# Optimization experiments

Hardware: AMD Instinct MI355X
Metric: run time of the kernel (lower is better)

Reference implementation:

```python
import jax, jax.numpy as jnp
import numpy as np

HEADS = 4
HID = 610
KER = 50  # cov2KerSize
NEG_SLOPE = 0.2


def gat_layer(x, src, dst, w, b, att_src, att_dst, n_nodes):
    # x: [N, Fin], w: [HEADS*HID, Fin], att_*: [1, HEADS, HID], b: [HID]
    h = (x @ w.T).reshape(n_nodes, HEADS, HID)               # [N,H,D]
    a_src = (h * att_src).sum(-1)                            # [N,H]
    a_dst = (h * att_dst).sum(-1)                            # [N,H]
    alpha = jax.nn.leaky_relu(a_src[src] + a_dst[dst], NEG_SLOPE)  # [E,H]
    # softmax over edges grouped by destination node
    m = jax.ops.segment_max(alpha, dst, num_segments=n_nodes)
    e = jnp.exp(alpha - m[dst])
    denom = jax.ops.segment_sum(e, dst, num_segments=n_nodes)
    a = e / (denom[dst] + 1e-16)                             # [E,H]
    msg = h[src] * a[:, :, None]                             # [E,H,D]
    out = jax.ops.segment_sum(msg, dst, num_segments=n_nodes)  # [N,H,D]
    return out.mean(axis=1) + b                              # [N,D] (concat=False)


def setup_inputs() -> dict:
    key = jax.random.key(0)
    ks = jax.random.split(key, 16)
    N, E, FIN, NOUT = 20000, 100000, 128, 86
    x = jax.random.normal(ks[0], (N, FIN), dtype=jnp.float32)
    edge_index = jax.random.randint(ks[1], (2, E), 0, N, dtype=jnp.int64)
    def kaiming(k, shape, fan_in):
        return jax.random.normal(k, shape, dtype=jnp.float32) * np.float32(np.sqrt(2.0 / fan_in))
    w0 = kaiming(ks[2], (HEADS * HID, FIN), FIN)
    b0 = jnp.zeros((HID,), jnp.float32)
    att_src0 = kaiming(ks[3], (1, HEADS, HID), HID)
    att_dst0 = kaiming(ks[4], (1, HEADS, HID), HID)
    w2 = kaiming(ks[5], (HEADS * HID, HID), HID)
    b2 = jnp.zeros((HID,), jnp.float32)
    att_src1 = kaiming(ks[6], (1, HEADS, HID), HID)
    att_dst1 = kaiming(ks[7], (1, HEADS, HID), HID)
    w4 = kaiming(ks[8], (1, 1, 2, KER), 2 * KER)
    b4 = jnp.zeros((1,), jnp.float32)
    w6 = kaiming(ks[9], (1, 1, KER), KER)
    b6 = jnp.zeros((1,), jnp.float32)
    w8 = kaiming(ks[10], (NOUT, 512), 512)
    b8 = jnp.zeros((NOUT,), jnp.float32)
    return dict(x=x, edge_index=edge_index, w0=w0, b0=b0, att_src0=att_src0,
                att_dst0=att_dst0, w2=w2, b2=b2, att_src1=att_src1,
                att_dst1=att_dst1, w4=w4, b4=b4, w6=w6, b6=b6, w8=w8, b8=b8)


def reference(x, edge_index, w0, b0, att_src0, att_dst0, w2, b2, att_src1,
              att_dst1, w4, b4, w6, b6, w8, b8):
    N = x.shape[0]
    src, dst = edge_index[0], edge_index[1]
    x1 = jax.nn.relu(gat_layer(x, src, dst, w0, b0, att_src0, att_dst0, N))
    x2 = jax.nn.relu(gat_layer(x1, src, dst, w2, b2, att_src1, att_dst1, N))
    # edge features: cat(src_feat, dst_feat) viewed as [E,1,2,HID]
    ef = jnp.stack([x2[src], x2[dst]], axis=1)[:, None, :, :]  # [E,1,2,HID]
    y = jax.lax.conv_general_dilated(ef, w4, (1, 1), 'VALID',
                                     dimension_numbers=('NCHW', 'OIHW', 'NCHW'))
    y = jax.nn.relu(y + b4[None, :, None, None])               # [E,1,1,561]
    y = y.reshape(-1, HID - KER + 1, 1).transpose(0, 2, 1)     # [E,1,561]
    y = jax.lax.conv_general_dilated(y, w6, (1,), 'VALID',
                                     dimension_numbers=('NCH', 'OIH', 'NCH'))
    y = jax.nn.relu(y + b6[None, :, None])                     # [E,1,512]
    # adaptive_avg_pool1d to 512 is identity since length is already 512
    y = y.reshape(-1, 512)
    return y @ w8.T + b8                                       # [E, num_outputs]
```

## Files before the change

kernel.cpp:

```cpp
#include <hip/hip_runtime.h>
#include <math.h>

#define HEADS 4
#define HID 610
#define HIDP 640
#define FIN 128
#define KER 50
#define NOUT 86
#define NEG_SLOPE 0.2f

#define Y1S 616
#define ZSS 520

typedef short bf8_t __attribute__((ext_vector_type(8)));
typedef float f4_t __attribute__((ext_vector_type(4)));

__device__ __forceinline__ ushort f2bf(float f) {
    unsigned u = __float_as_uint(f);
    unsigned r = (u + 0x7FFFu + ((u >> 16) & 1u)) >> 16;
    return (ushort)r;
}
__device__ __forceinline__ ushort f2bf_t(float f) {
    return (ushort)(__float_as_uint(f) >> 16);
}
__device__ __forceinline__ float bf2f(ushort b) { return __uint_as_float(((unsigned)b) << 16); }

__global__ void fill_val(float* __restrict__ p, float v, long n) {
    long i = (long)blockIdx.x * blockDim.x + threadIdx.x;
    if (i < n) p[i] = v;
}

__global__ void copy_int(const int* __restrict__ a, int* __restrict__ b, int n) {
    int i = blockIdx.x * blockDim.x + threadIdx.x;
    if (i < n) b[i] = a[i];
}

__global__ void hist_k(const int* __restrict__ ei, int* __restrict__ hist, int E) {
    int e = blockIdx.x * blockDim.x + threadIdx.x;
    if (e < E) atomicAdd(&hist[ei[E + e]], 1);
}

__global__ __launch_bounds__(1024) void scan_k(const int* __restrict__ hist,
                                               int* __restrict__ base, int Nn) {
    __shared__ int tmp[1024];
    __shared__ int carry;
    if (threadIdx.x == 0) carry = 0;
    __syncthreads();
    for (int c0 = 0; c0 < Nn; c0 += 1024) {
        int i = c0 + threadIdx.x;
        int v = (i < Nn) ? hist[i] : 0;
        tmp[threadIdx.x] = v;
        __syncthreads();
        for (int off = 1; off < 1024; off <<= 1) {
            int t = (threadIdx.x >= off) ? tmp[threadIdx.x - off] : 0;
            __syncthreads();
            tmp[threadIdx.x] += t;
            __syncthreads();
        }
        if (i < Nn) base[i] = carry + tmp[threadIdx.x] - v;
        __syncthreads();
        if (threadIdx.x == 1023) carry += tmp[1023];
        __syncthreads();
    }
    if (threadIdx.x == 0) base[Nn] = carry;
}

__global__ void scatter_k(const int* __restrict__ ei, int* __restrict__ cursor,
                          int* __restrict__ esrc, int* __restrict__ edst,
                          int* __restrict__ eorg, int E) {
    int e = blockIdx.x * blockDim.x + threadIdx.x;
    if (e >= E) return;
    int d = ei[E + e];
    int pos = atomicAdd(&cursor[d], 1);
    esrc[pos] = ei[e];
    edst[pos] = d;
    eorg[pos] = e;
}

__global__ void split_pad(const float* __restrict__ in, ushort* __restrict__ hi,
                          ushort* __restrict__ lo, int R, int K, int Kp) {
    long i = (long)blockIdx.x * blockDim.x + threadIdx.x;
    if (i >= (long)R * Kp) return;
    int r = (int)(i / Kp), c = (int)(i % Kp);
    float v = (c < K) ? in[(long)r * K + c] : 0.f;
    ushort h = f2bf(v);
    hi[i] = h;
    lo[i] = f2bf(v - bf2f(h));
}

__global__ void build_toeplitz(const float* __restrict__ w4, const float* __restrict__ w6,
                               ushort* __restrict__ T) {
    int i = blockIdx.x * blockDim.x + threadIdx.x;
    if (i >= 18 * 512) return;
    int e = i & 7;
    int lane = (i >> 3) & 63;
    int f = i >> 9;
    int n = lane & 15;
    int k = ((lane >> 4) << 3) + e;
    float wv;
    int hilo;
    if (f < 12) {
        int c = f % 3, hc = f / 3;
        int ch = hc & 1;
        hilo = hc >> 1;
        int d = c * 32 + k - n;
        wv = (d >= 0 && d < KER) ? w4[ch * KER + d] : 0.f;
    } else {
        int r2 = f - 12;
        int c = r2 % 3;
        hilo = r2 / 3;
        int d = c * 32 + k - n;
        wv = (d >= 0 && d < KER) ? w6[d] : 0.f;
    }
    ushort h = f2bf(wv);
    T[i] = hilo ? f2bf(wv - bf2f(h)) : h;
}

template <int AMODE, bool BIAS>
__global__ __launch_bounds__(256) void gemm_mfma(const float* __restrict__ A,
                                                 const ushort* __restrict__ Aghi,
                                                 const ushort* __restrict__ Aglo,
                                                 const ushort* __restrict__ Bghi,
                                                 const ushort* __restrict__ Bglo,
                                                 const float* __restrict__ bias,
                                                 float* __restrict__ C,
                                                 int M, int N, int Kp) {
    __shared__ __align__(16) ushort Ah[128 * 32];
    __shared__ __align__(16) ushort Al[128 * 32];
    __shared__ __align__(16) ushort Bh[128 * 32];
    __shared__ __align__(16) ushort Bl[128 * 32];
    int tid = threadIdx.x;
    int wave = tid >> 6, lane = tid & 63;
    int quad = lane >> 4, l16 = lane & 15;
    int wm = wave & 1, wn = wave >> 1;
    int row0 = blockIdx.y * 128, col0 = blockIdx.x * 128;

    float4 pa0[4];
    uint4 pah[2], pal[2], pbh[2], pbl[2];

    auto loadA = [&](int k0) {
        if (AMODE == 0) {
#pragma unroll
            for (int q = 0; q < 4; q++) {
                int p = tid + q * 256;
                int r = p >> 3, c4 = (p & 7) << 2;
                int gr = row0 + r;
                pa0[q] = (gr < M) ? *(const float4*)(A + (size_t)gr * Kp + k0 + c4)
                                  : make_float4(0.f, 0.f, 0.f, 0.f);
            }
        } else {
#pragma unroll
            for (int q = 0; q < 2; q++) {
                int p = tid + q * 256;
                int r = p >> 2, c = p & 3;
                int gr = row0 + r;
                if (gr < M) {
                    pah[q] = *(const uint4*)(Aghi + (size_t)gr * Kp + k0 + c * 8);
                    pal[q] = *(const uint4*)(Aglo + (size_t)gr * Kp + k0 + c * 8);
                } else {
                    pah[q] = make_uint4(0, 0, 0, 0);
                    pal[q] = make_uint4(0, 0, 0, 0);
                }
            }
        }
    };
    auto loadB = [&](int k0) {
#pragma unroll
        for (int q = 0; q < 2; q++) {
            int p = tid + q * 256;
            int r = p >> 2, c = p & 3;
            int gr = col0 + r;
            if (gr < N) {
                pbh[q] = *(const uint4*)(Bghi + (size_t)gr * Kp + k0 + c * 8);
                pbl[q] = *(const uint4*)(Bglo + (size_t)gr * Kp + k0 + c * 8);
            } else {
                pbh[q] = make_uint4(0, 0, 0, 0);
                pbl[q] = make_uint4(0, 0, 0, 0);
            }
        }
    };
    auto writeLDS = [&]() {
        if (AMODE == 0) {
#pragma unroll
            for (int q = 0; q < 4; q++) {
                int p = tid + q * 256;
                int r = p >> 3, m = p & 7;
                int pos = r * 32 + ((((m >> 1)) ^ ((r >> 1) & 3)) << 3) + ((m & 1) << 2);
                float4 v = pa0[q];
                ushort4 hv, lv;
                hv.x = f2bf(v.x); lv.x = f2bf(v.x - bf2f(hv.x));
                hv.y = f2bf(v.y); lv.y = f2bf(v.y - bf2f(hv.y));
                hv.z = f2bf(v.z); lv.z = f2bf(v.z - bf2f(hv.z));
                hv.w = f2bf(v.w); lv.w = f2bf(v.w - bf2f(hv.w));
                *(ushort4*)&Ah[pos] = hv;
                *(ushort4*)&Al[pos] = lv;
            }
        } else {
#pragma unroll
            for (int q = 0; q < 2; q++) {
                int p = tid + q * 256;
                int r = p >> 2, c = p & 3;
                int pos = r * 32 + ((c ^ ((r >> 1) & 3)) << 3);
                *(uint4*)&Ah[pos] = pah[q];
                *(uint4*)&Al[pos] = pal[q];
            }
        }
#pragma unroll
        for (int q = 0; q < 2; q++) {
            int p = tid + q * 256;
            int r = p >> 2, c = p & 3;
            int pos = r * 32 + ((c ^ ((r >> 1) & 3)) << 3);
            *(uint4*)&Bh[pos] = pbh[q];
            *(uint4*)&Bl[pos] = pbl[q];
        }
    };

    f4_t acc[4][4];
#pragma unroll
    for (int i = 0; i < 4; i++)
#pragma unroll
        for (int j = 0; j < 4; j++) acc[i][j] = (f4_t){0.f, 0.f, 0.f, 0.f};

    loadA(0);
    loadB(0);
    int sw = (quad ^ ((l16 >> 1) & 3)) << 3;
    for (int k0 = 0; k0 < Kp; k0 += 32) {
        __syncthreads();
        writeLDS();
        __syncthreads();
        if (k0 + 32 < Kp) {
            loadA(k0 + 32);
            loadB(k0 + 32);
        }
        bf8_t ah[4], al[4], bh[4], bl[4];
#pragma unroll
        for (int t = 0; t < 4; t++) {
            int ar = wm * 64 + t * 16 + l16;
            ah[t] = *(const bf8_t*)&Ah[ar * 32 + sw];
            al[t] = *(const bf8_t*)&Al[ar * 32 + sw];
            int br = wn * 64 + t * 16 + l16;
            bh[t] = *(const bf8_t*)&Bh[br * 32 + sw];
            bl[t] = *(const bf8_t*)&Bl[br * 32 + sw];
        }
#pragma unroll
        for (int i = 0; i < 4; i++)
#pragma unroll
            for (int j = 0; j < 4; j++) {
                acc[i][j] = __builtin_amdgcn_mfma_f32_16x16x32_bf16(ah[i], bh[j], acc[i][j], 0, 0, 0);
                acc[i][j] = __builtin_amdgcn_mfma_f32_16x16x32_bf16(al[i], bh[j], acc[i][j], 0, 0, 0);
                acc[i][j] = __builtin_amdgcn_mfma_f32_16x16x32_bf16(ah[i], bl[j], acc[i][j], 0, 0, 0);
            }
    }
#pragma unroll
    for (int i = 0; i < 4; i++) {
#pragma unroll
        for (int r = 0; r < 4; r++) {
            int grow = row0 + wm * 64 + i * 16 + quad * 4 + r;
            if (grow >= M) continue;
#pragma unroll
            for (int j = 0; j < 4; j++) {
                int gcol = col0 + wn * 64 + j * 16 + l16;
                if (gcol >= N) continue;
                float v = acc[i][j][r];
                if (BIAS) v += bias[gcol];
                C[(size_t)grow * N + gcol] = v;
            }
        }
    }
}

__global__ __launch_bounds__(256) void attn_dots(const float* __restrict__ h,
                                                 const float* __restrict__ att_s,
                                                 const float* __restrict__ att_d,
                                                 float* __restrict__ a_src,
                                                 float* __restrict__ a_dst, int Nn) {
    int n = blockIdx.x;
    int head = threadIdx.x >> 6;
    int lane = threadIdx.x & 63;
    const float2* hr = (const float2*)(h + (long)n * (HEADS * HID) + head * HID);
    const float2* as = (const float2*)(att_s + head * HID);
    const float2* ad = (const float2*)(att_d + head * HID);
    float ss = 0.f, sd = 0.f;
    for (int d = lane; d < HID / 2; d += 64) {
        float2 hv = hr[d], av = as[d], dv = ad[d];
        ss += hv.x * av.x + hv.y * av.y;
        sd += hv.x * dv.x + hv.y * dv.y;
    }
    for (int off = 32; off > 0; off >>= 1) {
        ss += __shfl_down(ss, off);
        sd += __shfl_down(sd, off);
    }
    if (lane == 0) {
        a_src[n * HEADS + head] = ss;
        a_dst[n * HEADS + head] = sd;
    }
}

template <int OUTMODE>
__global__ __launch_bounds__(256) void node_aggregate(
    const float* __restrict__ h, const float* __restrict__ asrc,
    const float* __restrict__ adst, const int* __restrict__ base,
    const int* __restrict__ esrc, const float* __restrict__ bias,
    float* __restrict__ xout, ushort* __restrict__ xhi, ushort* __restrict__ xlo,
    int Nn) {
    int wave = threadIdx.x >> 6, lane = threadIdx.x & 63;
    int n = blockIdx.x * 4 + wave;
    if (n >= Nn) return;
    int b0 = base[n], deg = base[n + 1] - b0;
    float ad[HEADS];
#pragma unroll
    for (int hh = 0; hh < HEADS; hh++) ad[hh] = adst[n * HEADS + hh];
    float m[HEADS] = {-INFINITY, -INFINITY, -INFINITY, -INFINITY};
    for (int eb = 0; eb < deg; eb += 64) {
        int i = eb + lane;
        if (i < deg) {
            int s = esrc[b0 + i];
#pragma unroll
            for (int hh = 0; hh < HEADS; hh++) {
                float v = asrc[s * HEADS + hh] + ad[hh];
                v = v >= 0.f ? v : NEG_SLOPE * v;
                m[hh] = fmaxf(m[hh], v);
            }
        }
    }
#pragma unroll
    for (int off = 32; off > 0; off >>= 1)
#pragma unroll
        for (int hh = 0; hh < HEADS; hh++) m[hh] = fmaxf(m[hh], __shfl_xor(m[hh], off));
    float sden[HEADS] = {0.f, 0.f, 0.f, 0.f};
    for (int eb = 0; eb < deg; eb += 64) {
        int i = eb + lane;
        if (i < deg) {
            int s = esrc[b0 + i];
#pragma unroll
            for (int hh = 0; hh < HEADS; hh++) {
                float v = asrc[s * HEADS + hh] + ad[hh];
                v = v >= 0.f ? v : NEG_SLOPE * v;
                sden[hh] += expf(v - m[hh]);
            }
        }
    }
#pragma unroll
    for (int off = 32; off > 0; off >>= 1)
#pragma unroll
        for (int hh = 0; hh < HEADS; hh++) sden[hh] += __shfl_xor(sden[hh], off);
    float inv[HEADS];
#pragma unroll
    for (int hh = 0; hh < HEADS; hh++) inv[hh] = 0.25f / (sden[hh] + 1e-16f);
    float acc0[10] = {}, acc1[10] = {}, acc2[10] = {}, acc3[10] = {};
    for (int eb = 0; eb < deg; eb += 64) {
        int i = eb + lane;
        int sreg = 0;
        float coef[HEADS] = {0.f, 0.f, 0.f, 0.f};
        if (i < deg) {
            sreg = esrc[b0 + i];
#pragma unroll
            for (int hh = 0; hh < HEADS; hh++) {
                float v = asrc[sreg * HEADS + hh] + ad[hh];
                v = v >= 0.f ? v : NEG_SLOPE * v;
                coef[hh] = expf(v - m[hh]) * inv[hh];
            }
        }
        int cnt = deg - eb < 64 ? deg - eb : 64;
        for (int j = 0; j < cnt; j++) {
            int s = __shfl(sreg, j);
            float c0 = __shfl(coef[0], j), c1 = __shfl(coef[1], j);
            float c2 = __shfl(coef[2], j), c3 = __shfl(coef[3], j);
            const float* hr = h + (size_t)s * (HEADS * HID);
#pragma unroll
            for (int t = 0; t < 10; t++) {
                int d = lane + t * 64;
                if (d < HID) {
                    acc0[t] = fmaf(c0, hr[d], acc0[t]);
                    acc1[t] = fmaf(c1, hr[HID + d], acc1[t]);
                    acc2[t] = fmaf(c2, hr[2 * HID + d], acc2[t]);
                    acc3[t] = fmaf(c3, hr[3 * HID + d], acc3[t]);
                }
            }
        }
    }
#pragma unroll
    for (int t = 0; t < 10; t++) {
        int d = lane + t * 64;
        if (d < HID) {
            float v = acc0[t] + acc1[t] + acc2[t] + acc3[t] + bias[d];
            v = v > 0.f ? v : 0.f;
            if (OUTMODE == 0) {
                xout[(size_t)n * HIDP + d] = v;
            } else {
                ushort hv = f2bf(v);
                xhi[(size_t)n * HIDP + d] = hv;
                xlo[(size_t)n * HIDP + d] = f2bf(v - bf2f(hv));
            }
        }
    }
    for (int d = HID + lane; d < HIDP; d += 64) {
        if (OUTMODE == 0) {
            xout[(size_t)n * HIDP + d] = 0.f;
        } else {
            xhi[(size_t)n * HIDP + d] = 0;
            xlo[(size_t)n * HIDP + d] = 0;
        }
    }
}

__global__ __launch_bounds__(256, 3) void edge_fused(
    const ushort* __restrict__ x2hi, const ushort* __restrict__ x2lo,
    const int* __restrict__ esrc, const int* __restrict__ edst,
    const int* __restrict__ eorg, const ushort* __restrict__ T,
    const float* __restrict__ b4, const float* __restrict__ b6,
    const ushort* __restrict__ w8hi, const ushort* __restrict__ w8lo,
    const float* __restrict__ b8, float* __restrict__ out, int E) {
    __shared__ __align__(16) ushort y1h[16 * Y1S];
    __shared__ __align__(16) ushort y1l[16 * Y1S];
    const int tid = threadIdx.x;
    const int wave = tid >> 6, lane = tid & 63;
    const int quad = lane >> 4, l16 = lane & 15;
    const int e0 = blockIdx.x * 16;
    const int p = wave & 1;
    const int half = wave >> 1;
    const int p16 = p * 16;

    int i = e0 + l16;
    if (i >= E) i = E - 1;
    const int s = esrc[i], d = edst[i];
    const ushort* psh = x2hi + (size_t)s * HIDP + quad * 8;
    const ushort* psl = x2lo + (size_t)s * HIDP + quad * 8;
    const ushort* pth = x2hi + (size_t)d * HIDP + quad * 8;
    const ushort* ptl = x2lo + (size_t)d * HIDP + quad * 8;

    bf8_t Wsh[6], Wsl[6], Wth[6], Wtl[6];
#define LDCH(slot, m)                                     \
    {                                                     \
        const int o_ = p16 + 32 * (m);                    \
        Wsh[slot] = *(const bf8_t*)(psh + o_);            \
        Wth[slot] = *(const bf8_t*)(pth + o_);            \
        if ((m) <= 18) {                                  \
            Wsl[slot] = *(const bf8_t*)(psl + o_);        \
            Wtl[slot] = *(const bf8_t*)(ptl + o_);        \
        }                                                 \
    }
    const int t0 = half * 9;
#pragma unroll
    for (int m = 0; m < 5; m++) LDCH(m, t0 + m);

    for (int idx = tid; idx < 16 * (Y1S - 576); idx += 256) {
        int r = idx / (Y1S - 576);
        int j = 576 + (idx - r * (Y1S - 576));
        y1h[r * Y1S + j] = 0;
        y1l[r * Y1S + j] = 0;
    }

    bf8_t B1h[2][3], B1l[2][2];
#pragma unroll
    for (int ch = 0; ch < 2; ch++) {
#pragma unroll
        for (int c = 0; c < 3; c++)
            B1h[ch][c] = *(const bf8_t*)&T[(ch * 3 + c) * 512 + lane * 8];
#pragma unroll
        for (int c = 0; c < 2; c++)
            B1l[ch][c] = *(const bf8_t*)&T[((2 + ch) * 3 + c) * 512 + lane * 8];
    }
    const float bb4 = b4[0], bb6 = b6[0];

#pragma unroll
    for (int tt = 0; tt < 9; tt++) {
        if (tt <= 5) LDCH((tt + 5) % 6, t0 + tt + 5);
        const int c0 = tt % 6, c1 = (tt + 1) % 6, c2 = (tt + 2) % 6;
        f4_t acc = {bb4, bb4, bb4, bb4};
        acc = __builtin_amdgcn_mfma_f32_16x16x32_bf16(Wsh[c0], B1h[0][0], acc, 0, 0, 0);
        acc = __builtin_amdgcn_mfma_f32_16x16x32_bf16(Wsl[c0], B1h[0][0], acc, 0, 0, 0);
        acc = __builtin_amdgcn_mfma_f32_16x16x32_bf16(Wsh[c0], B1l[0][0], acc, 0, 0, 0);
        acc = __builtin_amdgcn_mfma_f32_16x16x32_bf16(Wth[c0], B1h[1][0], acc, 0, 0, 0);
        acc = __builtin_amdgcn_mfma_f32_16x16x32_bf16(Wtl[c0], B1h[1][0], acc, 0, 0, 0);
        acc = __builtin_amdgcn_mfma_f32_16x16x32_bf16(Wth[c0], B1l[1][0], acc, 0, 0, 0);
        acc = __builtin_amdgcn_mfma_f32_16x16x32_bf16(Wsh[c1], B1h[0][1], acc, 0, 0, 0);
        acc = __builtin_amdgcn_mfma_f32_16x16x32_bf16(Wsl[c1], B1h[0][1], acc, 0, 0, 0);
        acc = __builtin_amdgcn_mfma_f32_16x16x32_bf16(Wsh[c1], B1l[0][1], acc, 0, 0, 0);
        acc = __builtin_amdgcn_mfma_f32_16x16x32_bf16(Wth[c1], B1h[1][1], acc, 0, 0, 0);
        acc = __builtin_amdgcn_mfma_f32_16x16x32_bf16(Wtl[c1], B1h[1][1], acc, 0, 0, 0);
        acc = __builtin_amdgcn_mfma_f32_16x16x32_bf16(Wth[c1], B1l[1][1], acc, 0, 0, 0);
        acc = __builtin_amdgcn_mfma_f32_16x16x32_bf16(Wsh[c2], B1h[0][2], acc, 0, 0, 0);
        acc = __builtin_amdgcn_mfma_f32_16x16x32_bf16(Wth[c2], B1h[1][2], acc, 0, 0, 0);
        const int j0 = p16 + 32 * (t0 + tt);
#pragma unroll
        for (int r = 0; r < 4; r++) {
            int e_ = quad * 4 + r;
            int pos = e_ * Y1S + j0 + l16;
            float v = acc[r];
            v = v > 0.f ? v : 0.f;
            ushort hh = f2bf_t(v);
            y1h[pos] = hh;
            y1l[pos] = f2bf(v - bf2f(hh));
        }
    }
    __syncthreads();

    bf8_t B2h[3], B2l[2];
#pragma unroll
    for (int c = 0; c < 3; c++) B2h[c] = *(const bf8_t*)&T[(12 + c) * 512 + lane * 8];
#pragma unroll
    for (int c = 0; c < 2; c++) B2l[c] = *(const bf8_t*)&T[(15 + c) * 512 + lane * 8];
    const int arow1 = l16 * Y1S + quad * 8;
    bf8_t Yh[4], Yl[4];
#define LDY(slot, m)                                          \
    {                                                         \
        const int o_ = arow1 + p16 + 32 * (m);                \
        Yh[slot] = *(const bf8_t*)&y1h[o_];                   \
        if ((m) <= 16) Yl[slot] = *(const bf8_t*)&y1l[o_];    \
    }
    const int t0b = half * 8;
#pragma unroll
    for (int m = 0; m < 3; m++) LDY(m, t0b + m);
    f4_t zac[8];
#pragma unroll
    for (int tt = 0; tt < 8; tt++) {
        if (tt <= 6) LDY((tt + 3) & 3, t0b + tt + 3);
        const int c0 = tt & 3, c1 = (tt + 1) & 3, c2 = (tt + 2) & 3;
        f4_t acc = {bb6, bb6, bb6, bb6};
        acc = __builtin_amdgcn_mfma_f32_16x16x32_bf16(Yh[c0], B2h[0], acc, 0, 0, 0);
        acc = __builtin_amdgcn_mfma_f32_16x16x32_bf16(Yl[c0], B2h[0], acc, 0, 0, 0);
        acc = __builtin_amdgcn_mfma_f32_16x16x32_bf16(Yh[c0], B2l[0], acc, 0, 0, 0);
        acc = __builtin_amdgcn_mfma_f32_16x16x32_bf16(Yh[c1], B2h[1], acc, 0, 0, 0);
        acc = __builtin_amdgcn_mfma_f32_16x16x32_bf16(Yl[c1], B2h[1], acc, 0, 0, 0);
        acc = __builtin_amdgcn_mfma_f32_16x16x32_bf16(Yh[c1], B2l[1], acc, 0, 0, 0);
        acc = __builtin_amdgcn_mfma_f32_16x16x32_bf16(Yh[c2], B2h[2], acc, 0, 0, 0);
#pragma unroll
        for (int r = 0; r < 4; r++) {
            float v = acc[r];
            zac[tt][r] = v > 0.f ? v : 0.f;
        }
    }
    __syncthreads();

#pragma unroll
    for (int tt = 0; tt < 8; tt++) {
        const int j02 = p16 + 32 * (t0b + tt);
#pragma unroll
        for (int r = 0; r < 4; r++) {
            int e_ = quad * 4 + r;
            int pos = e_ * ZSS + j02 + l16;
            float v = zac[tt][r];
            ushort hh = f2bf_t(v);
            y1h[pos] = hh;
            y1l[pos] = f2bf(v - bf2f(hh));
        }
    }
    __syncthreads();

#pragma unroll
    for (int it = 0; it < 2; it++) {
        const int nt = wave + it * 4;
        if (nt < 6) {
            const int col = nt * 16 + l16;
            const int wrow = col < NOUT ? col : 0;
            const float bias = col < NOUT ? b8[col] : 0.f;
            f4_t acc = {bias, bias, bias, bias};
            const int arow = l16 * ZSS + quad * 8;
            const ushort* wph = w8hi + (size_t)wrow * 512 + quad * 8;
            const ushort* wpl = w8lo + (size_t)wrow * 512 + quad * 8;
#pragma unroll
            for (int c = 0; c < 16; c++) {
                bf8_t zh = *(const bf8_t*)&y1h[arow + c * 32];
                bf8_t zl = *(const bf8_t*)&y1l[arow + c * 32];
                bf8_t wh = *(const bf8_t*)(wph + c * 32);
                bf8_t wl = *(const bf8_t*)(wpl + c * 32);
                acc = __builtin_amdgcn_mfma_f32_16x16x32_bf16(zh, wh, acc, 0, 0, 0);
                acc = __builtin_amdgcn_mfma_f32_16x16x32_bf16(zl, wh, acc, 0, 0, 0);
                acc = __builtin_amdgcn_mfma_f32_16x16x32_bf16(zh, wl, acc, 0, 0, 0);
            }
            if (col < NOUT) {
#pragma unroll
                for (int r = 0; r < 4; r++) {
                    int er = e0 + quad * 4 + r;
                    if (er < E) out[(size_t)eorg[er] * NOUT + col] = acc[r];
                }
            }
        }
    }
#undef LDCH
#undef LDY
}

extern "C" void kernel_launch(void* const* d_in, const int* in_sizes, int n_in,
                              void* d_out, int out_size, void* d_ws, size_t ws_size,
                              hipStream_t stream) {
    const float* x = (const float*)d_in[0];
    const int* ei = (const int*)d_in[1];
    const float* w0 = (const float*)d_in[2];
    const float* b0 = (const float*)d_in[3];
    const float* att_s0 = (const float*)d_in[4];
    const float* att_d0 = (const float*)d_in[5];
    const float* w2 = (const float*)d_in[6];
    const float* b2 = (const float*)d_in[7];
    const float* att_s1 = (const float*)d_in[8];
    const float* att_d1 = (const float*)d_in[9];
    const float* w4 = (const float*)d_in[10];
    const float* b4 = (const float*)d_in[11];
    const float* w6 = (const float*)d_in[12];
    const float* b6 = (const float*)d_in[13];
    const float* w8 = (const float*)d_in[14];
    const float* b8 = (const float*)d_in[15];
    float* out = (float*)d_out;

    const int Nn = in_sizes[0] / FIN;
    const int E = in_sizes[1] / 2;
    const int HD = HEADS * HID;

    float* ws = (float*)d_ws;
    size_t o = 0;
    float* buf1 = ws + o; o += (size_t)Nn * HIDP;
    ushort* x1hi = (ushort*)buf1;
    ushort* x1lo = x1hi + (size_t)Nn * HIDP;
    ushort* w8hi = (ushort*)(ws + o);
    ushort* w8lo = w8hi + (size_t)NOUT * 512; o += (size_t)NOUT * 512;
    int* base = (int*)(ws + o); o += (size_t)Nn + 4;
    int* cursor = (int*)(ws + o); o += (size_t)Nn;
    int* esrc = (int*)(ws + o); o += (size_t)E;
    int* edst = (int*)(ws + o); o += (size_t)E;
    int* eorg = (int*)(ws + o); o += (size_t)E;
    float* asrc = ws + o; o += (size_t)Nn * HEADS;
    float* adst = ws + o; o += (size_t)Nn * HEADS;
    ushort* w0hi = (ushort*)(ws + o);
    ushort* w0lo = w0hi + (size_t)HD * FIN; o += (size_t)HD * FIN;
    ushort* w2hi = (ushort*)(ws + o);
    ushort* w2lo = w2hi + (size_t)HD * HIDP; o += (size_t)HD * HIDP;
    float* h = ws + o;

    int edgeGrid = (E + 255) / 256;
    int nodeWaveGrid = (Nn + 3) / 4;
    int fusedGrid = (E + 15) / 16;
    dim3 gGemmL((HD + 127) / 128, (Nn + 127) / 128);

    split_pad<<<((HD * FIN) + 255) / 256, 256, 0, stream>>>(w0, w0hi, w0lo, HD, FIN, FIN);
    split_pad<<<((HD * HIDP) + 255) / 256, 256, 0, stream>>>(w2, w2hi, w2lo, HD, HID, HIDP);
    split_pad<<<((NOUT * 512) + 255) / 256, 256, 0, stream>>>(w8, w8hi, w8lo, NOUT, 512, 512);
    fill_val<<<(Nn + 255) / 256, 256, 0, stream>>>((float*)cursor, 0.f, Nn);
    hist_k<<<edgeGrid, 256, 0, stream>>>(ei, cursor, E);
    scan_k<<<1, 1024, 0, stream>>>(cursor, base, Nn);
    copy_int<<<(Nn + 255) / 256, 256, 0, stream>>>(base, cursor, Nn);
    scatter_k<<<edgeGrid, 256, 0, stream>>>(ei, cursor, esrc, edst, eorg, E);

    gemm_mfma<0, false><<<gGemmL, 256, 0, stream>>>(x, nullptr, nullptr, w0hi, w0lo, nullptr,
                                                    h, Nn, HD, FIN);
    build_toeplitz<<<(18 * 512 + 255) / 256, 256, 0, stream>>>(w4, w6, w0hi);
    attn_dots<<<Nn, 256, 0, stream>>>(h, att_s0, att_d0, asrc, adst, Nn);
    node_aggregate<1><<<nodeWaveGrid, 256, 0, stream>>>(h, asrc, adst, base, esrc, b0,
                                                        nullptr, x1hi, x1lo, Nn);

    gemm_mfma<1, false><<<gGemmL, 256, 0, stream>>>(nullptr, x1hi, x1lo, w2hi, w2lo, nullptr,
                                                    h, Nn, HD, HIDP);
    attn_dots<<<Nn, 256, 0, stream>>>(h, att_s1, att_d1, asrc, adst, Nn);
    node_aggregate<1><<<nodeWaveGrid, 256, 0, stream>>>(h, asrc, adst, base, esrc, b2,
                                                        nullptr, x1hi, x1lo, Nn);

    edge_fused<<<fusedGrid, 256, 0, stream>>>(x1hi, x1lo, esrc, edst, eorg, w0hi, b4, b6,
                                              w8hi, w8lo, b8, out, E);
}
```

Before: 1.054 ms.

## Use direct global-to-LDS loads in bf16 GEMM path and raise edge kernel occupancy

For the pre-split bf16 A-operand mode, the GEMM now issues global_load_lds 16-byte loads straight into swizzled shared memory instead of staging through registers. This removes register staging and the separate LDS write step. The trade-off is that register prefetch double-buffering is lost, so loads are no longer overlapped with compute, and the new path drops the M/N bounds checks. Separately, the edge_fused kernel's launch bounds minimum-blocks hint goes from 3 to 4 to push occupancy, which may cause register spills.

```diff
diff --git a/kernel.cpp b/kernel.cpp
--- a/kernel.cpp
+++ b/kernel.cpp
@@ -24,6 +24,11 @@
     return (ushort)(__float_as_uint(f) >> 16);
 }
 __device__ __forceinline__ float bf2f(ushort b) { return __uint_as_float(((unsigned)b) << 16); }
+
+__device__ __forceinline__ void gload16(const void* g, void* l) {
+    __builtin_amdgcn_global_load_lds((const __attribute__((address_space(1))) void*)g,
+                                     (__attribute__((address_space(3))) void*)l, 16, 0, 0);
+}
 
 __global__ void fill_val(float* __restrict__ p, float v, long n) {
     long i = (long)blockIdx.x * blockDim.x + threadIdx.x;
@@ -135,11 +140,38 @@
     int wm = wave & 1, wn = wave >> 1;
     int row0 = blockIdx.y * 128, col0 = blockIdx.x * 128;
 
-    float4 pa0[4];
-    uint4 pah[2], pal[2], pbh[2], pbl[2];
-
-    auto loadA = [&](int k0) {
-        if (AMODE == 0) {
+    f4_t acc[4][4];
+#pragma unroll
+    for (int i = 0; i < 4; i++)
+#pragma unroll
+        for (int j = 0; j < 4; j++) acc[i][j] = (f4_t){0.f, 0.f, 0.f, 0.f};
+
+    int sw = (quad ^ ((l16 >> 1) & 3)) << 3;
+    auto compute_tile = [&]() {
+        bf8_t ah[4], al[4], bh[4], bl[4];
+#pragma unroll
+        for (int t = 0; t < 4; t++) {
+            int ar = wm * 64 + t * 16 + l16;
+            ah[t] = *(const bf8_t*)&Ah[ar * 32 + sw];
+            al[t] = *(const bf8_t*)&Al[ar * 32 + sw];
+            int br = wn * 64 + t * 16 + l16;
+            bh[t] = *(const bf8_t*)&Bh[br * 32 + sw];
+            bl[t] = *(const bf8_t*)&Bl[br * 32 + sw];
+        }
+#pragma unroll
+        for (int i = 0; i < 4; i++)
+#pragma unroll
+            for (int j = 0; j < 4; j++) {
+                acc[i][j] = __builtin_amdgcn_mfma_f32_16x16x32_bf16(ah[i], bh[j], acc[i][j], 0, 0, 0);
+                acc[i][j] = __builtin_amdgcn_mfma_f32_16x16x32_bf16(al[i], bh[j], acc[i][j], 0, 0, 0);
+                acc[i][j] = __builtin_amdgcn_mfma_f32_16x16x32_bf16(ah[i], bl[j], acc[i][j], 0, 0, 0);
+            }
+    };
+
+    if constexpr (AMODE == 0) {
+        float4 pa0[4];
+        uint4 pbh[2], pbl[2];
+        auto loadA = [&](int k0) {
 #pragma unroll
             for (int q = 0; q < 4; q++) {
                 int p = tid + q * 256;
@@ -148,39 +180,23 @@
                 pa0[q] = (gr < M) ? *(const float4*)(A + (size_t)gr * Kp + k0 + c4)
                                   : make_float4(0.f, 0.f, 0.f, 0.f);
             }
-        } else {
+        };
+        auto loadB = [&](int k0) {
 #pragma unroll
             for (int q = 0; q < 2; q++) {
                 int p = tid + q * 256;
                 int r = p >> 2, c = p & 3;
-                int gr = row0 + r;
-                if (gr < M) {
-                    pah[q] = *(const uint4*)(Aghi + (size_t)gr * Kp + k0 + c * 8);
-                    pal[q] = *(const uint4*)(Aglo + (size_t)gr * Kp + k0 + c * 8);
+                int gr = col0 + r;
+                if (gr < N) {
+                    pbh[q] = *(const uint4*)(Bghi + (size_t)gr * Kp + k0 + c * 8);
+                    pbl[q] = *(const uint4*)(Bglo + (size_t)gr * Kp + k0 + c * 8);
                 } else {
-                    pah[q] = make_uint4(0, 0, 0, 0);
-                    pal[q] = make_uint4(0, 0, 0, 0);
+                    pbh[q] = make_uint4(0, 0, 0, 0);
+                    pbl[q] = make_uint4(0, 0, 0, 0);
                 }
             }
-        }
-    };
-    auto loadB = [&](int k0) {
-#pragma unroll
-        for (int q = 0; q < 2; q++) {
-            int p = tid + q * 256;
-            int r = p >> 2, c = p & 3;
-            int gr = col0 + r;
-            if (gr < N) {
-                pbh[q] = *(const uint4*)(Bghi + (size_t)gr * Kp + k0 + c * 8);
-                pbl[q] = *(const uint4*)(Bglo + (size_t)gr * Kp + k0 + c * 8);
-            } else {
-                pbh[q] = make_uint4(0, 0, 0, 0);
-                pbl[q] = make_uint4(0, 0, 0, 0);
-            }
-        }
-    };
-    auto writeLDS = [&]() {
-        if (AMODE == 0) {
+        };
+        auto writeLDS = [&]() {
 #pragma unroll
             for (int q = 0; q < 4; q++) {
                 int p = tid + q * 256;
@@ -195,62 +211,48 @@
                 *(ushort4*)&Ah[pos] = hv;
                 *(ushort4*)&Al[pos] = lv;
             }
-        } else {
 #pragma unroll
             for (int q = 0; q < 2; q++) {
                 int p = tid + q * 256;
                 int r = p >> 2, c = p & 3;
                 int pos = r * 32 + ((c ^ ((r >> 1) & 3)) << 3);
-                *(uint4*)&Ah[pos] = pah[q];
-                *(uint4*)&Al[pos] = pal[q];
-            }
-        }
-#pragma unroll
-        for (int q = 0; q < 2; q++) {
-            int p = tid + q * 256;
-            int r = p >> 2, c = p & 3;
-            int pos = r * 32 + ((c ^ ((r >> 1) & 3)) << 3);
-            *(uint4*)&Bh[pos] = pbh[q];
-            *(uint4*)&Bl[pos] = pbl[q];
-        }
-    };
-
-    f4_t acc[4][4];
-#pragma unroll
-    for (int i = 0; i < 4; i++)
-#pragma unroll
-        for (int j = 0; j < 4; j++) acc[i][j] = (f4_t){0.f, 0.f, 0.f, 0.f};
-
-    loadA(0);
-    loadB(0);
-    int sw = (quad ^ ((l16 >> 1) & 3)) << 3;
-    for (int k0 = 0; k0 < Kp; k0 += 32) {
-        __syncthreads();
-        writeLDS();
-        __syncthreads();
-        if (k0 + 32 < Kp) {
-            loadA(k0 + 32);
-            loadB(k0 + 32);
-        }
-        bf8_t ah[4], al[4], bh[4], bl[4];
-#pragma unroll
-        for (int t = 0; t < 4; t++) {
-            int ar = wm * 64 + t * 16 + l16;
-            ah[t] = *(const bf8_t*)&Ah[ar * 32 + sw];
-            al[t] = *(const bf8_t*)&Al[ar * 32 + sw];
-            int br = wn * 64 + t * 16 + l16;
-            bh[t] = *(const bf8_t*)&Bh[br * 32 + sw];
-            bl[t] = *(const bf8_t*)&Bl[br * 32 + sw];
-        }
-#pragma unroll
-        for (int i = 0; i < 4; i++)
-#pragma unroll
-            for (int j = 0; j < 4; j++) {
-                acc[i][j] = __builtin_amdgcn_mfma_f32_16x16x32_bf16(ah[i], bh[j], acc[i][j], 0, 0, 0);
-                acc[i][j] = __builtin_amdgcn_mfma_f32_16x16x32_bf16(al[i], bh[j], acc[i][j], 0, 0, 0);
-                acc[i][j] = __builtin_amdgcn_mfma_f32_16x16x32_bf16(ah[i], bl[j], acc[i][j], 0, 0, 0);
-            }
-    }
+                *(uint4*)&Bh[pos] = pbh[q];
+                *(uint4*)&Bl[pos] = pbl[q];
+            }
+        };
+        loadA(0);
+        loadB(0);
+        for (int k0 = 0; k0 < Kp; k0 += 32) {
+            __syncthreads();
+            writeLDS();
+            __syncthreads();
+            if (k0 + 32 < Kp) {
+                loadA(k0 + 32);
+                loadB(k0 + 32);
+            }
+            compute_tile();
+        }
+    } else {
+        const int r_ = lane >> 2, cs = lane & 3;
+        for (int k0 = 0; k0 < Kp; k0 += 32) {
+            __syncthreads();
+#pragma unroll
+            for (int q = 0; q < 2; q++) {
+                const int r0 = wave * 32 + q * 16;
+                const int r = r0 + r_;
+                const int ca = cs ^ ((r >> 1) & 3);
+                const size_t goA = (size_t)(row0 + r) * Kp + k0 + ca * 8;
+                const size_t goB = (size_t)(col0 + r) * Kp + k0 + ca * 8;
+                gload16(Aghi + goA, &Ah[r0 * 32]);
+                gload16(Aglo + goA, &Al[r0 * 32]);
+                gload16(Bghi + goB, &Bh[r0 * 32]);
+                gload16(Bglo + goB, &Bl[r0 * 32]);
+            }
+            __syncthreads();
+            compute_tile();
+        }
+    }
+
 #pragma unroll
     for (int i = 0; i < 4; i++) {
 #pragma unroll
@@ -404,7 +406,7 @@
     }
 }
 
-__global__ __launch_bounds__(256, 3) void edge_fused(
+__global__ __launch_bounds__(256, 4) void edge_fused(
     const ushort* __restrict__ x2hi, const ushort* __restrict__ x2lo,
     const int* __restrict__ esrc, const int* __restrict__ edst,
     const int* __restrict__ eorg, const ushort* __restrict__ T,
```

New measurement: 1.180 ms. 12.0% more time.
